# Kernel tuning notes

Measured on AMD Instinct MI355X. Metric: run time of the kernel, lower is better.

The kernel has to match this reference:

```python
import jax, jax.numpy as jnp
import numpy as np

B, T, C, H, W_SP = 16, 256, 1024, 8, 8
OUT = 1024
ALPHA_INIT = 0.9


def setup_inputs() -> dict:
    key = jax.random.key(0)
    k_x, k_w = jax.random.split(key, 2)
    x = jax.random.normal(k_x, (B, T, C, H, W_SP), dtype=jnp.float32)
    r0 = jnp.zeros((B, OUT), dtype=jnp.float32)
    W = jax.random.normal(k_w, (OUT, C), dtype=jnp.float32) * 0.02
    b = jnp.zeros((OUT,), dtype=jnp.float32)
    alpha = jnp.full((OUT,), ALPHA_INIT, dtype=jnp.float32)
    return {"x": x, "r0": r0, "W": W, "b": b, "alpha": alpha}


def reference(x, r0, W, b, alpha):
    # x: [B, T, C, H, W] -> spatial mean -> [B, T, C]
    xm = x.mean(axis=(3, 4))
    # per-timestep linear done as one batched matmul: [B, T, OUT]
    u = jnp.einsum('btc,oc->bto', xm, W) + b
    # linear diagonal recurrence r_t = alpha * r_{t-1} + u_t
    def step(r, u_t):
        r = alpha * r + u_t
        return r, r
    r_final, r_seq = jax.lax.scan(step, r0, jnp.swapaxes(u, 0, 1))  # scan over T
    r_seq = jnp.swapaxes(r_seq, 0, 1)  # [B, T, OUT]
    return (r_seq, r_final)
```

## Files before the change

kernel.cpp:

```cpp
#include <hip/hip_runtime.h>
#include <hip/hip_bf16.h>
#include <stdint.h>


typedef __attribute__((ext_vector_type(8))) short bf16x8;
typedef __attribute__((ext_vector_type(4))) float f32x4;

__device__ __forceinline__ unsigned short f2bf(float f) {
  union { float f; unsigned int u; } c; c.f = f;
  unsigned int u = c.u;
  return (unsigned short)((u + 0x7FFFu + ((u >> 16) & 1u)) >> 16);
}

__global__ __launch_bounds__(256) void k_mean(const float* __restrict__ x,
                                              unsigned short* __restrict__ xm,
                                              const float* __restrict__ W,
                                              unsigned short* __restrict__ Wb) {
  const int tid = threadIdx.x;
  const int wi = blockIdx.x * 256 + tid;
  if (wi < 262144) {
    float4 v = *(const float4*)(W + wi * 4);
    ushort4 o;
    o.x = f2bf(v.x); o.y = f2bf(v.y); o.z = f2bf(v.z); o.w = f2bf(v.w);
    *(ushort4*)(Wb + wi * 4) = o;
  }
  const int sub = tid & 15;
  const int grp = tid >> 4;
  for (int base = blockIdx.x * 16; base < (1 << 22); base += gridDim.x * 16) {
    int seg = base + grp;
    const float4 v = *(const float4*)(x + (long)seg * 64 + sub * 4);
    float s = v.x + v.y + v.z + v.w;
    s += __shfl_xor(s, 1);
    s += __shfl_xor(s, 2);
    s += __shfl_xor(s, 4);
    s += __shfl_xor(s, 8);
    if (sub == 0) xm[seg] = f2bf(s * 0.015625f);
  }
}

#define GLDS16(g, l) \
  __builtin_amdgcn_global_load_lds((const __attribute__((address_space(1))) void*)(g), \
                                   (__attribute__((address_space(3))) void*)(l), 16, 0, 0)

__global__ __launch_bounds__(256) void k_gemm(const unsigned short* __restrict__ A,
                                              const unsigned short* __restrict__ Bm,
                                              const float* __restrict__ bias,
                                              float* __restrict__ U) {
  __shared__ unsigned short lds[2][12288];
  const int bid = blockIdx.x;
  const int nb  = (bid & 7) * 64 + (bid >> 3);
  const int m0  = (nb >> 4) * 128;
  const int n0  = (nb & 15) * 64;

  const int tid  = threadIdx.x;
  const int lane = tid & 63;
  const int wid  = tid >> 6;
  const int wr = wid >> 1, wc = wid & 1;

  f32x4 acc[4][2] = {};

  const int srow8  = tid >> 3;
  const int sslot8 = tid & 7;
  const int gkoff  = (sslot8 ^ (srow8 & 7)) << 3;
  const int r16    = lane & 15;
  const int kb     = lane >> 4;

  const unsigned short* ag[4];
  const unsigned short* bg[2];
#pragma unroll
  for (int ra = 0; ra < 4; ra++) ag[ra] = A  + (long)(m0 + ra * 32 + srow8) * 1024 + gkoff;
#pragma unroll
  for (int rb = 0; rb < 2; rb++) bg[rb] = Bm + (long)(n0 + rb * 32 + srow8) * 1024 + gkoff;

  auto stage = [&](int t) {
    const int k0 = t * 64;
    char* Ab = (char*)&lds[t & 1][0];
    char* Bb = (char*)&lds[t & 1][8192];
#pragma unroll
    for (int ra = 0; ra < 4; ra++) GLDS16(ag[ra] + k0, Ab + tid * 16 + ra * 4096);
#pragma unroll
    for (int rb = 0; rb < 2; rb++) GLDS16(bg[rb] + k0, Bb + tid * 16 + rb * 4096);
  };

  auto compute = [&](int t) {
    const unsigned short* Ab = &lds[t & 1][0];
    const unsigned short* Bb = &lds[t & 1][8192];
    bf16x8 af[2][4], bf_[2][2];
#pragma unroll
    for (int ks = 0; ks < 2; ks++) {
#pragma unroll
      for (int i = 0; i < 4; i++) {
        const int rr = wr * 64 + i * 16 + r16;
        af[ks][i] = *(const bf16x8*)(Ab + rr * 64 + (((ks * 4 + kb) ^ (rr & 7)) << 3));
      }
#pragma unroll
      for (int j = 0; j < 2; j++) {
        const int cc = wc * 32 + j * 16 + r16;
        bf_[ks][j] = *(const bf16x8*)(Bb + cc * 64 + (((ks * 4 + kb) ^ (cc & 7)) << 3));
      }
    }
#pragma unroll
    for (int ks = 0; ks < 2; ks++)
#pragma unroll
      for (int i = 0; i < 4; i++)
#pragma unroll
        for (int j = 0; j < 2; j++)
          acc[i][j] = __builtin_amdgcn_mfma_f32_16x16x32_bf16(af[ks][i], bf_[ks][j], acc[i][j], 0, 0, 0);
  };

  stage(0);
  __syncthreads();
#pragma unroll 1
  for (int t = 0; t < 16; t++) {
    if (t < 15) stage(t + 1);
    compute(t);
    __syncthreads();
  }

  const int orow = (lane >> 4) * 4;
  const int ocol = lane & 15;
  const float bb[2] = { bias[n0 + wc * 32 + ocol], bias[n0 + wc * 32 + 16 + ocol] };
#pragma unroll
  for (int i = 0; i < 4; i++)
#pragma unroll
    for (int j = 0; j < 2; j++) {
      const int m = m0 + wr * 64 + i * 16 + orow;
      const int n = n0 + wc * 32 + j * 16 + ocol;
#pragma unroll
      for (int q = 0; q < 4; q++)
        U[(long)(m + q) * 1024 + n] = acc[i][j][q] + bb[j];
    }
}

template<int G>
__device__ __forceinline__ void scan_load(float* buf, const float* p) {
#pragma unroll
  for (int i = 0; i < 64; i++) buf[i] = p[G * 65536 + i * 1024];
}
template<int G>
__device__ __forceinline__ void scan_proc(float* buf, float* p, float a, float& r) {
#pragma unroll
  for (int i = 0; i < 64; i++) { r = fmaf(a, r, buf[i]); buf[i] = r; }
#pragma unroll
  for (int i = 0; i < 64; i++) p[G * 65536 + i * 1024] = buf[i];
}

__global__ __launch_bounds__(64) void k_scan(const float* __restrict__ r0,
                                             const float* __restrict__ alpha,
                                             float* __restrict__ out) {
  const int gid = blockIdx.x * 64 + threadIdx.x;
  const int o = gid & 1023;
  const float a = alpha[o];
  float r = r0[gid];
  float* p = out + (long)(gid >> 10) * (256L * 1024) + o;
  float bufA[64], bufB[64];
  scan_load<0>(bufA, p);
  scan_load<1>(bufB, p); scan_proc<0>(bufA, p, a, r);
  scan_load<2>(bufA, p); scan_proc<1>(bufB, p, a, r);
  scan_load<3>(bufB, p); scan_proc<2>(bufA, p, a, r);
  scan_proc<3>(bufB, p, a, r);
  out[(1 << 22) + gid] = r;
}

extern "C" void kernel_launch(void* const* d_in, const int* in_sizes, int n_in,
                              void* d_out, int out_size, void* d_ws, size_t ws_size,
                              hipStream_t stream) {
  const float* x     = (const float*)d_in[0];
  const float* r0    = (const float*)d_in[1];
  const float* W     = (const float*)d_in[2];
  const float* b     = (const float*)d_in[3];
  const float* alpha = (const float*)d_in[4];
  float* out = (float*)d_out;

  unsigned short* xm = (unsigned short*)d_ws;
  unsigned short* Wb = (unsigned short*)((char*)d_ws + (8u << 20));

  k_mean<<<2048, 256, 0, stream>>>(x, xm, W, Wb);
  k_gemm<<<512, 256, 0, stream>>>(xm, Wb, b, out);
  k_scan<<<256, 64, 0, stream>>>(r0, alpha, out);
}
```

Measured before the change: 231.1 us.

## Fuse recurrence scan into GEMM epilogue with per-tile parallel prefix scan

Removes the separate scan kernel by folding the linear recurrence into the GEMM epilogue. Each block now owns a full batch's 256 timesteps for 64 output columns. It runs a parallel prefix scan across MFMA accumulator rows using lane shuffles and precomputed powers of alpha, then carries the state across waves through LDS. This avoids writing u to memory and reading it back for the scan, and drops one kernel launch. In exchange the grid halves to 256 blocks with larger tiles (launch bounds set to one block per CU). The reassociated power-based scan may also change floating-point rounding slightly.

```diff
diff --git a/kernel.cpp b/kernel.cpp
--- a/kernel.cpp
+++ b/kernel.cpp
@@ -42,60 +42,63 @@
   __builtin_amdgcn_global_load_lds((const __attribute__((address_space(1))) void*)(g), \
                                    (__attribute__((address_space(3))) void*)(l), 16, 0, 0)
 
-__global__ __launch_bounds__(256) void k_gemm(const unsigned short* __restrict__ A,
-                                              const unsigned short* __restrict__ Bm,
-                                              const float* __restrict__ bias,
-                                              float* __restrict__ U) {
-  __shared__ unsigned short lds[2][12288];
+__global__ __launch_bounds__(256, 1) void k_gemmscan(const unsigned short* __restrict__ A,
+                                                     const unsigned short* __restrict__ Bm,
+                                                     const float* __restrict__ bias,
+                                                     const float* __restrict__ r0,
+                                                     const float* __restrict__ alpha,
+                                                     float* __restrict__ out) {
+  __shared__ unsigned short lds[2][20480];
   const int bid = blockIdx.x;
-  const int nb  = (bid & 7) * 64 + (bid >> 3);
-  const int m0  = (nb >> 4) * 128;
+  const int nb  = (bid & 7) * 32 + (bid >> 3);
+  const int b   = nb >> 4;
   const int n0  = (nb & 15) * 64;
+  const int m0  = b * 256;
 
   const int tid  = threadIdx.x;
   const int lane = tid & 63;
-  const int wid  = tid >> 6;
-  const int wr = wid >> 1, wc = wid & 1;
-
-  f32x4 acc[4][2] = {};
+  const int w    = tid >> 6;
+  const int r16  = lane & 15;
+  const int kb   = lane >> 4;
+  const int h    = lane >> 4;
+
+  f32x4 acc[4][4] = {};
 
   const int srow8  = tid >> 3;
   const int sslot8 = tid & 7;
   const int gkoff  = (sslot8 ^ (srow8 & 7)) << 3;
-  const int r16    = lane & 15;
-  const int kb     = lane >> 4;
-
-  const unsigned short* ag[4];
+
+  const unsigned short* ag[8];
   const unsigned short* bg[2];
 #pragma unroll
-  for (int ra = 0; ra < 4; ra++) ag[ra] = A  + (long)(m0 + ra * 32 + srow8) * 1024 + gkoff;
+  for (int ra = 0; ra < 8; ra++) ag[ra] = A  + (long)(m0 + ra * 32 + srow8) * 1024 + gkoff;
 #pragma unroll
   for (int rb = 0; rb < 2; rb++) bg[rb] = Bm + (long)(n0 + rb * 32 + srow8) * 1024 + gkoff;
 
   auto stage = [&](int t) {
     const int k0 = t * 64;
     char* Ab = (char*)&lds[t & 1][0];
-    char* Bb = (char*)&lds[t & 1][8192];
-#pragma unroll
-    for (int ra = 0; ra < 4; ra++) GLDS16(ag[ra] + k0, Ab + tid * 16 + ra * 4096);
+    char* Bb = (char*)&lds[t & 1][16384];
+#pragma unroll
+    for (int ra = 0; ra < 8; ra++) GLDS16(ag[ra] + k0, Ab + tid * 16 + ra * 4096);
 #pragma unroll
     for (int rb = 0; rb < 2; rb++) GLDS16(bg[rb] + k0, Bb + tid * 16 + rb * 4096);
   };
 
   auto compute = [&](int t) {
     const unsigned short* Ab = &lds[t & 1][0];
-    const unsigned short* Bb = &lds[t & 1][8192];
-    bf16x8 af[2][4], bf_[2][2];
+    const unsigned short* Bb = &lds[t & 1][16384];
+    bf16x8 af[2][4], bf_[2][4];
 #pragma unroll
     for (int ks = 0; ks < 2; ks++) {
 #pragma unroll
       for (int i = 0; i < 4; i++) {
-        const int rr = wr * 64 + i * 16 + r16;
+        const int rr = w * 64 + i * 16 + r16;
         af[ks][i] = *(const bf16x8*)(Ab + rr * 64 + (((ks * 4 + kb) ^ (rr & 7)) << 3));
       }
 #pragma unroll
-      for (int j = 0; j < 2; j++) {
-        const int cc = wc * 32 + j * 16 + r16;
+      for (int j = 0; j < 4; j++) {
+        const int cc = j * 16 + r16;
         bf_[ks][j] = *(const bf16x8*)(Bb + cc * 64 + (((ks * 4 + kb) ^ (cc & 7)) << 3));
       }
     }
@@ -104,7 +107,7 @@
 #pragma unroll
       for (int i = 0; i < 4; i++)
 #pragma unroll
-        for (int j = 0; j < 2; j++)
+        for (int j = 0; j < 4; j++)
           acc[i][j] = __builtin_amdgcn_mfma_f32_16x16x32_bf16(af[ks][i], bf_[ks][j], acc[i][j], 0, 0, 0);
   };
 
@@ -117,49 +120,77 @@
     __syncthreads();
   }
 
-  const int orow = (lane >> 4) * 4;
-  const int ocol = lane & 15;
-  const float bb[2] = { bias[n0 + wc * 32 + ocol], bias[n0 + wc * 32 + 16 + ocol] };
+  float a1[4], a2[4], a3[4], a4[4], a8[4], a12[4], a16[4], a64[4], p4h[4], r0v[4], Cw[4];
+#pragma unroll
+  for (int j = 0; j < 4; j++) {
+    const int col = n0 + j * 16 + r16;
+    const float a = alpha[col];
+    a1[j] = a; a2[j] = a * a; a3[j] = a2[j] * a; a4[j] = a2[j] * a2[j];
+    a8[j] = a4[j] * a4[j]; a12[j] = a8[j] * a4[j]; a16[j] = a8[j] * a8[j];
+    const float a32 = a16[j] * a16[j]; a64[j] = a32 * a32;
+    p4h[j] = (h == 0) ? 1.f : (h == 1) ? a4[j] : (h == 2) ? a8[j] : a12[j];
+    r0v[j] = r0[b * 1024 + col];
+    const float bb = bias[col];
+    Cw[j] = 0.f;
+#pragma unroll
+    for (int i = 0; i < 4; i++) {
+      const float u0 = acc[i][j][0] + bb, u1 = acc[i][j][1] + bb;
+      const float u2 = acc[i][j][2] + bb, u3 = acc[i][j][3] + bb;
+      const float l0 = u0;
+      const float l1 = fmaf(a1[j], l0, u1);
+      const float l2 = fmaf(a1[j], l1, u2);
+      const float l3 = fmaf(a1[j], l2, u3);
+      float xv = l3;
+      float t1 = __shfl_up(xv, 16); if (h >= 1) xv = fmaf(a4[j], t1, xv);
+      float t2 = __shfl_up(xv, 32); if (h >= 2) xv = fmaf(a8[j], t2, xv);
+      float P  = __shfl_up(xv, 16); if (h == 0) P = 0.f;
+      const float G = fmaf(p4h[j], Cw[j], P);
+      acc[i][j][0] = fmaf(a1[j], G, l0);
+      acc[i][j][1] = fmaf(a2[j], G, l1);
+      acc[i][j][2] = fmaf(a3[j], G, l2);
+      acc[i][j][3] = fmaf(a4[j], G, l3);
+      const float xe = __shfl(xv, r16 + 48);
+      Cw[j] = fmaf(a16[j], Cw[j], xe);
+    }
+  }
+
+  float* F = (float*)&lds[0][0];
+  if (h == 0) {
+#pragma unroll
+    for (int j = 0; j < 4; j++) F[w * 64 + j * 16 + r16] = Cw[j];
+  }
+  __syncthreads();
+  float R[4];
+#pragma unroll
+  for (int j = 0; j < 4; j++) {
+    R[j] = r0v[j];
+    for (int v = 0; v < w; v++) R[j] = fmaf(a64[j], R[j], F[v * 64 + j * 16 + r16]);
+    float gi = p4h[j] * R[j];
+#pragma unroll
+    for (int i = 0; i < 4; i++) {
+      acc[i][j][0] = fmaf(a1[j], gi, acc[i][j][0]);
+      acc[i][j][1] = fmaf(a2[j], gi, acc[i][j][1]);
+      acc[i][j][2] = fmaf(a3[j], gi, acc[i][j][2]);
+      acc[i][j][3] = fmaf(a4[j], gi, acc[i][j][3]);
+      gi *= a16[j];
+    }
+  }
+
 #pragma unroll
   for (int i = 0; i < 4; i++)
 #pragma unroll
-    for (int j = 0; j < 2; j++) {
-      const int m = m0 + wr * 64 + i * 16 + orow;
-      const int n = n0 + wc * 32 + j * 16 + ocol;
+    for (int j = 0; j < 4; j++) {
+      const long mrow = m0 + w * 64 + i * 16 + h * 4;
+      const int  n    = n0 + j * 16 + r16;
 #pragma unroll
       for (int q = 0; q < 4; q++)
-        U[(long)(m + q) * 1024 + n] = acc[i][j][q] + bb[j];
-    }
-}
-
-template<int G>
-__device__ __forceinline__ void scan_load(float* buf, const float* p) {
-#pragma unroll
-  for (int i = 0; i < 64; i++) buf[i] = p[G * 65536 + i * 1024];
-}
-template<int G>
-__device__ __forceinline__ void scan_proc(float* buf, float* p, float a, float& r) {
-#pragma unroll
-  for (int i = 0; i < 64; i++) { r = fmaf(a, r, buf[i]); buf[i] = r; }
-#pragma unroll
-  for (int i = 0; i < 64; i++) p[G * 65536 + i * 1024] = buf[i];
-}
-
-__global__ __launch_bounds__(64) void k_scan(const float* __restrict__ r0,
-                                             const float* __restrict__ alpha,
-                                             float* __restrict__ out) {
-  const int gid = blockIdx.x * 64 + threadIdx.x;
-  const int o = gid & 1023;
-  const float a = alpha[o];
-  float r = r0[gid];
-  float* p = out + (long)(gid >> 10) * (256L * 1024) + o;
-  float bufA[64], bufB[64];
-  scan_load<0>(bufA, p);
-  scan_load<1>(bufB, p); scan_proc<0>(bufA, p, a, r);
-  scan_load<2>(bufA, p); scan_proc<1>(bufB, p, a, r);
-  scan_load<3>(bufB, p); scan_proc<2>(bufA, p, a, r);
-  scan_proc<3>(bufB, p, a, r);
-  out[(1 << 22) + gid] = r;
+        out[(mrow + q) * 1024 + n] = acc[i][j][q];
+    }
+  if (w == 3 && h == 0) {
+#pragma unroll
+    for (int j = 0; j < 4; j++)
+      out[(1 << 22) + b * 1024 + n0 + j * 16 + r16] = fmaf(a64[j], R[j], F[192 + j * 16 + r16]);
+  }
 }
 
 extern "C" void kernel_launch(void* const* d_in, const int* in_sizes, int n_in,
@@ -176,6 +207,5 @@
   unsigned short* Wb = (unsigned short*)((char*)d_ws + (8u << 20));
 
   k_mean<<<2048, 256, 0, stream>>>(x, xm, W, Wb);
-  k_gemm<<<512, 256, 0, stream>>>(xm, Wb, b, out);
-  k_scan<<<256, 64, 0, stream>>>(r0, alpha, out);
-}
+  k_gemmscan<<<256, 256, 0, stream>>>(xm, Wb, b, r0, alpha, out);
+}
```

Result: no change. 228.3 us (-1.2%).
